# Optimization experiments

Measured on AMD Instinct MI355X. Metric: run time of the kernel, lower is better.

## Reference

```python
import jax, jax.numpy as jnp
import numpy as np

NUM_HEADS = 8
CHUNK = 64


def setup_inputs() -> dict:
    key = jax.random.key(0)
    k1, k2, k3, k4 = jax.random.split(key, 4)
    B, C, H, W = 16, 384, 64, 64
    x = jax.random.normal(k1, (B, C, H, W), dtype=jnp.float32)
    # torch nn.Linear weights are [out, in]; qkv has no bias (qkv_bias=False)
    qkv_w = jax.random.normal(k2, (3 * C, C), dtype=jnp.float32) * (C ** -0.5)
    proj_w = jax.random.normal(k3, (C, C), dtype=jnp.float32) * (C ** -0.5)
    proj_b = jax.random.normal(k4, (C,), dtype=jnp.float32) * 0.02
    return {"x": x, "qkv_w": qkv_w, "proj_w": proj_w, "proj_b": proj_b}


def reference(x, qkv_w, proj_w, proj_b):
    B, C, H, W = x.shape
    N = H * W
    nh = NUM_HEADS
    hd = C // nh
    scale = hd ** -0.5
    nc = N // CHUNK  # number of non-overlapping local blocks

    t = x.reshape(B, C, N).transpose(0, 2, 1)  # [B, N, C]
    qkv = t @ qkv_w.T  # [B, N, 3C]
    qkv = qkv.reshape(B, N, 3, nh, hd).transpose(2, 0, 3, 1, 4)  # [3, B, nh, N, hd]
    q, k, v = qkv[0], qkv[1], qkv[2]

    # block-local attention: reshape N -> (nc, CHUNK) and batch over blocks
    q = q.reshape(B, nh, nc, CHUNK, hd)
    k = k.reshape(B, nh, nc, CHUNK, hd)
    v = v.reshape(B, nh, nc, CHUNK, hd)

    scores = jnp.einsum('bhnqd,bhnkd->bhnqk', q, k) * scale  # [B,nh,nc,CHUNK,CHUNK]
    attn = jax.nn.softmax(scores, axis=-1)
    out = jnp.einsum('bhnqk,bhnkd->bhnqd', attn, v)  # [B,nh,nc,CHUNK,hd]

    out = out.reshape(B, nh, N, hd).transpose(0, 2, 1, 3).reshape(B, N, C)
    out = out @ proj_w.T + proj_b
    return out.transpose(0, 2, 1).reshape(B, C, H, W)
```

## Files before the change

kernel.cpp:

```cpp
#include <hip/hip_runtime.h>
#include <stdint.h>

#define NH 8
#define HD 48
#define CC 384
#define NN 4096
#define CK 384

typedef short short8 __attribute__((ext_vector_type(8)));
typedef float floatx4 __attribute__((ext_vector_type(4)));

__device__ inline unsigned short f32_to_bf16_bits(float f) {
    uint32_t u = __builtin_bit_cast(uint32_t, f);
    u = (u + 0x7FFFu + ((u >> 16) & 1u)) >> 16;
    return (unsigned short)u;
}
__device__ inline short8 load8(const unsigned short* p) {
    return *reinterpret_cast<const short8*>(p);
}
typedef __attribute__((address_space(1))) const void gvoid_t;
typedef __attribute__((address_space(3))) void lvoid_t;
__device__ inline void async16(const unsigned short* g, unsigned short* l) {
    __builtin_amdgcn_global_load_lds((gvoid_t*)g, (lvoid_t*)l, 16, 0, 0);
}

__global__ __launch_bounds__(256) void k_cvt(
    const float* __restrict__ src, unsigned short* __restrict__ dst, int n8)
{
    int i = blockIdx.x * 256 + threadIdx.x;
    if (i >= n8) return;
    const float* s = src + (size_t)i * 8;
    unsigned short t[8];
    #pragma unroll
    for (int j = 0; j < 8; ++j) t[j] = f32_to_bf16_bits(s[j]);
    *reinterpret_cast<short8*>(dst + (size_t)i * 8) = *reinterpret_cast<short8*>(t);
}

__global__ __launch_bounds__(256) void k_tr(
    const float* __restrict__ x, unsigned short* __restrict__ xT)
{
    __shared__ unsigned short tile[64][72];
    int bx = blockIdx.x;
    int nt = bx & 63; int rest = bx >> 6; int ct = rest % 6; int b = rest / 6;
    int c0 = ct * 64, n0 = nt * 64;
    int t = threadIdx.x;
    int nl = t & 63, w = t >> 6;
    const float* xb = x + (size_t)b * CC * NN;
    #pragma unroll
    for (int i = 0; i < 4; ++i) {
        int cl = w * 16 + i * 4;
        unsigned short u[4];
        #pragma unroll
        for (int j = 0; j < 4; ++j)
            u[j] = f32_to_bf16_bits(xb[(size_t)(c0 + cl + j) * NN + n0 + nl]);
        *reinterpret_cast<uint2*>(&tile[nl][cl]) = *reinterpret_cast<uint2*>(u);
    }
    __syncthreads();
    #pragma unroll
    for (int it = 0; it < 2; ++it) {
        int v = it * 256 + t;
        int row = v >> 3, seg = v & 7;
        *reinterpret_cast<short8*>(xT + ((size_t)b * NN + n0 + row) * CK + c0 + seg * 8) =
            load8(&tile[row][seg * 8]);
    }
}

__global__ __launch_bounds__(256) void k_qkv(
    const unsigned short* __restrict__ A,
    const unsigned short* __restrict__ W,
    unsigned short* __restrict__ QK,
    unsigned short* __restrict__ Vt)
{
    __shared__ unsigned short smem[17408];
    int bx = blockIdx.x;
    int l  = (bx & 7) * 576 + (bx >> 3);
    int tf = l % 9, tm = l / 9;
    int m0 = tm * 128, f0 = tf * 128;
    int tid = threadIdx.x, wid = tid >> 6, lane = tid & 63;
    int l15 = lane & 15, quad = lane >> 4;
    int wm = wid & 1, wn = wid >> 1;

    const unsigned short* Ab = A + (size_t)m0 * CK;
    const unsigned short* Wb = W + (size_t)f0 * CK;

    floatx4 acc[4][4] = {};

    auto stage = [&](int kt, int buf) {
        int k0 = kt * 32;
        unsigned short* Asd = smem + buf * 8192;
        unsigned short* Wsd = Asd + 4096;
        #pragma unroll
        for (int i = 0; i < 2; ++i) {
            int c = i * 256 + tid;
            int row = c >> 2;
            int sg  = (c & 3) ^ (row & 3);
            async16(Ab + (size_t)row * CK + k0 + sg * 8, Asd + (i * 256 + wid * 64) * 8);
            async16(Wb + (size_t)row * CK + k0 + sg * 8, Wsd + (i * 256 + wid * 64) * 8);
        }
    };

    stage(0, 0);
    __syncthreads();

    int sx = (quad ^ (l15 & 3)) * 8;
    int cur = 0;
    #pragma unroll
    for (int kk = 0; kk < 12; ++kk) {
        if (kk < 11) stage(kk + 1, cur ^ 1);
        unsigned short* As = smem + cur * 8192;
        unsigned short* Ws = As + 4096;
        short8 a[4], bf[4];
        #pragma unroll
        for (int i = 0; i < 4; ++i)
            a[i] = load8(As + (wm * 64 + i * 16 + l15) * 32 + sx);
        #pragma unroll
        for (int j = 0; j < 4; ++j)
            bf[j] = load8(Ws + (wn * 64 + j * 16 + l15) * 32 + sx);
        #pragma unroll
        for (int i = 0; i < 4; ++i)
            #pragma unroll
            for (int j = 0; j < 4; ++j)
                acc[i][j] = __builtin_amdgcn_mfma_f32_16x16x32_bf16(a[i], bf[j], acc[i][j], 0, 0, 0);
        __syncthreads();
        cur ^= 1;
    }

    int b = m0 >> 12, nb = m0 & 4095;
    if (tf < 6) {
        #pragma unroll
        for (int i = 0; i < 4; ++i)
            #pragma unroll
            for (int j = 0; j < 4; ++j)
                #pragma unroll
                for (int r = 0; r < 4; ++r)
                    smem[(wm * 64 + i * 16 + quad * 4 + r) * 128 + wn * 64 + j * 16 + l15] =
                        f32_to_bf16_bits(acc[i][j][r]);
        __syncthreads();
        #pragma unroll
        for (int it = 0; it < 8; ++it) {
            int c = it * 256 + tid;
            int row = c >> 4, seg = c & 15;
            *reinterpret_cast<short8*>(QK + (size_t)(m0 + row) * 768 + f0 + seg * 8) =
                load8(smem + row * 128 + seg * 8);
        }
    } else {
        #pragma unroll
        for (int i = 0; i < 4; ++i)
            #pragma unroll
            for (int j = 0; j < 4; ++j)
                #pragma unroll
                for (int r = 0; r < 4; ++r)
                    smem[(wn * 64 + j * 16 + l15) * 136 + wm * 64 + i * 16 + quad * 4 + r] =
                        f32_to_bf16_bits(acc[i][j][r]);
        __syncthreads();
        int fvb = (tf - 6) * 128;
        #pragma unroll
        for (int it = 0; it < 8; ++it) {
            int c = it * 256 + tid;
            int fl = c >> 4, seg = c & 15;
            int fv = fvb + fl;
            int h = fv / 48, d = fv - h * 48;
            *reinterpret_cast<short8*>(Vt + (((size_t)(b * 8 + h) * 48 + d) << 12) + nb + seg * 8) =
                load8(smem + fl * 136 + seg * 8);
        }
    }
}

__global__ __launch_bounds__(256) void k_attn(
    const unsigned short* __restrict__ QK,
    const unsigned short* __restrict__ Vt,
    unsigned short* __restrict__ AO)
{
    __shared__ unsigned short ql[64][72];
    __shared__ unsigned short kl[64][72];
    __shared__ unsigned short vt[48][72];
    __shared__ float          sc[64][66];
    __shared__ unsigned short pl[64][72];

    int bx = blockIdx.x;
    int cn = bx & 63, h = (bx >> 6) & 7, b = bx >> 9;
    int n0 = cn * 64;
    int tid = threadIdx.x, wid = tid >> 6, lane = tid & 63;
    int l15 = lane & 15, quad = lane >> 4;
    int m0w = wid * 16;
    int h48 = h * 48;
    size_t b4 = (size_t)b * NN + n0;

    for (int v = tid; v < 768; v += 256) {
        int mat = v / 384;
        int idx = v - mat * 384;
        int rr = idx / 6, seg = idx - rr * 6;
        uint4 val = *reinterpret_cast<const uint4*>(QK + (b4 + rr) * 768 + mat * 384 + h48 + seg * 8);
        unsigned short* dst = mat ? &kl[rr][seg * 8] : &ql[rr][seg * 8];
        *reinterpret_cast<uint4*>(dst) = val;
    }
    {
        short8 z = {};
        int v = tid;
        if (v < 256) {
            int mat = v >> 7, rr = (v >> 1) & 63, half = v & 1;
            unsigned short* dst = mat ? &kl[rr][48 + half * 8] : &ql[rr][48 + half * 8];
            *reinterpret_cast<short8*>(dst) = z;
        }
    }
    for (int v = tid; v < 384; v += 256) {
        int d = v >> 3, seg = v & 7;
        *reinterpret_cast<uint4*>(&vt[d][seg * 8]) =
            *reinterpret_cast<const uint4*>(Vt + (((size_t)(b * 8 + h) * 48 + d) << 12) + n0 + seg * 8);
    }
    __syncthreads();

    const float scale = 0.14433756729740643f;
    #pragma unroll
    for (int t = 0; t < 4; ++t) {
        floatx4 sacc = {};
        #pragma unroll
        for (int ks = 0; ks < 2; ++ks) {
            short8 a  = load8(&ql[m0w + l15][ks * 32 + quad * 8]);
            short8 bb = load8(&kl[t * 16 + l15][ks * 32 + quad * 8]);
            sacc = __builtin_amdgcn_mfma_f32_16x16x32_bf16(a, bb, sacc, 0, 0, 0);
        }
        #pragma unroll
        for (int r = 0; r < 4; ++r)
            sc[m0w + quad * 4 + r][t * 16 + l15] = sacc[r] * scale;
    }
    __syncthreads();

    {
        int row = m0w + l15;
        int jb  = quad * 16;
        float ev[16];
        #pragma unroll
        for (int jj = 0; jj < 16; ++jj) ev[jj] = sc[row][jb + jj];
        float m = ev[0];
        #pragma unroll
        for (int jj = 1; jj < 16; ++jj) m = fmaxf(m, ev[jj]);
        m = fmaxf(m, __shfl_xor(m, 16));
        m = fmaxf(m, __shfl_xor(m, 32));
        float s = 0.f;
        #pragma unroll
        for (int jj = 0; jj < 16; ++jj) { ev[jj] = __expf(ev[jj] - m); s += ev[jj]; }
        s += __shfl_xor(s, 16);
        s += __shfl_xor(s, 32);
        float inv = 1.0f / s;
        #pragma unroll
        for (int jj = 0; jj < 16; ++jj) pl[row][jb + jj] = f32_to_bf16_bits(ev[jj] * inv);
    }
    __syncthreads();

    #pragma unroll
    for (int t = 0; t < 3; ++t) {
        floatx4 oacc = {};
        #pragma unroll
        for (int ks = 0; ks < 2; ++ks) {
            short8 a  = load8(&pl[m0w + l15][ks * 32 + quad * 8]);
            short8 bb = load8(&vt[t * 16 + l15][ks * 32 + quad * 8]);
            oacc = __builtin_amdgcn_mfma_f32_16x16x32_bf16(a, bb, oacc, 0, 0, 0);
        }
        #pragma unroll
        for (int r = 0; r < 4; ++r)
            kl[m0w + quad * 4 + r][t * 16 + l15] = f32_to_bf16_bits(oacc[r]);
    }
    __syncthreads();

    for (int v = tid; v < 384; v += 256) {
        int rr = v / 6, seg = v - rr * 6;
        *reinterpret_cast<short8*>(AO + (b4 + rr) * CC + h48 + seg * 8) =
            load8(&kl[rr][seg * 8]);
    }
}

__global__ __launch_bounds__(256) void k_proj(
    const unsigned short* __restrict__ A,
    const unsigned short* __restrict__ W,
    const float* __restrict__ bias,
    float* __restrict__ out)
{
    __shared__ unsigned short smem[17408];
    float* fs = (float*)smem;
    int bx = blockIdx.x;
    int l  = (bx & 7) * 192 + (bx >> 3);
    int tf = l % 3, tm = l / 3;
    int m0 = tm * 128, f0 = tf * 128;
    int tid = threadIdx.x, wid = tid >> 6, lane = tid & 63;
    int l15 = lane & 15, quad = lane >> 4;
    int wm = wid & 1, wn = wid >> 1;

    const unsigned short* Ab = A + (size_t)m0 * CK;
    const unsigned short* Wb = W + (size_t)f0 * CK;

    floatx4 acc[4][4] = {};

    auto stage = [&](int kt, int buf) {
        int k0 = kt * 32;
        unsigned short* Asd = smem + buf * 8192;
        unsigned short* Wsd = Asd + 4096;
        #pragma unroll
        for (int i = 0; i < 2; ++i) {
            int c = i * 256 + tid;
            int row = c >> 2;
            int sg  = (c & 3) ^ (row & 3);
            async16(Ab + (size_t)row * CK + k0 + sg * 8, Asd + (i * 256 + wid * 64) * 8);
            async16(Wb + (size_t)row * CK + k0 + sg * 8, Wsd + (i * 256 + wid * 64) * 8);
        }
    };

    stage(0, 0);
    __syncthreads();

    int sx = (quad ^ (l15 & 3)) * 8;
    int cur = 0;
    #pragma unroll
    for (int kk = 0; kk < 12; ++kk) {
        if (kk < 11) stage(kk + 1, cur ^ 1);
        unsigned short* As = smem + cur * 8192;
        unsigned short* Ws = As + 4096;
        short8 a[4], bf[4];
        #pragma unroll
        for (int i = 0; i < 4; ++i)
            a[i] = load8(As + (wm * 64 + i * 16 + l15) * 32 + sx);
        #pragma unroll
        for (int j = 0; j < 4; ++j)
            bf[j] = load8(Ws + (wn * 64 + j * 16 + l15) * 32 + sx);
        #pragma unroll
        for (int i = 0; i < 4; ++i)
            #pragma unroll
            for (int j = 0; j < 4; ++j)
                acc[i][j] = __builtin_amdgcn_mfma_f32_16x16x32_bf16(a[i], bf[j], acc[i][j], 0, 0, 0);
        __syncthreads();
        cur ^= 1;
    }

    int b = m0 >> 12, nb = m0 & 4095;
    #pragma unroll
    for (int hh = 0; hh < 2; ++hh) {
        if (wn == hh) {
            #pragma unroll
            for (int j = 0; j < 4; ++j) {
                float bv = bias[f0 + hh * 64 + j * 16 + l15];
                #pragma unroll
                for (int i = 0; i < 4; ++i)
                    #pragma unroll
                    for (int r = 0; r < 4; ++r)
                        fs[(j * 16 + l15) * 132 + wm * 64 + i * 16 + quad * 4 + r] =
                            acc[i][j][r] + bv;
            }
        }
        __syncthreads();
        #pragma unroll
        for (int it = 0; it < 8; ++it) {
            int c = it * 256 + tid;
            int cl = c >> 5, seg = c & 31;
            *reinterpret_cast<float4*>(
                out + (((size_t)(b * CC + f0 + hh * 64 + cl)) << 12) + nb + seg * 4) =
                *reinterpret_cast<const float4*>(fs + cl * 132 + seg * 4);
        }
        __syncthreads();
    }
}

extern "C" void kernel_launch(void* const* d_in, const int* in_sizes, int n_in,
                              void* d_out, int out_size, void* d_ws, size_t ws_size,
                              hipStream_t stream) {
    const float* x      = (const float*)d_in[0];
    const float* qkv_w  = (const float*)d_in[1];
    const float* proj_w = (const float*)d_in[2];
    const float* proj_b = (const float*)d_in[3];
    float* out = (float*)d_out;

    const size_t nX  = (size_t)16 * CC * NN;
    const size_t nW1 = (size_t)3 * CC * CC;
    const size_t nW2 = (size_t)CC * CC;

    unsigned short* xT  = (unsigned short*)d_ws;
    unsigned short* w1b = xT  + nX;
    unsigned short* w2b = w1b + nW1;
    unsigned short* QK  = w2b + nW2;
    unsigned short* Vt  = QK  + (size_t)16 * NN * 768;
    unsigned short* AO  = Vt  + (size_t)16 * 8 * 48 * NN;

    k_tr  <<<dim3(16 * 6 * 64), dim3(256), 0, stream>>>(x, xT);
    k_cvt <<<dim3((int)(nW1 / 8 + 255) / 256), dim3(256), 0, stream>>>(qkv_w, w1b, (int)(nW1 / 8));
    k_cvt <<<dim3((int)(nW2 / 8 + 255) / 256), dim3(256), 0, stream>>>(proj_w, w2b, (int)(nW2 / 8));

    k_qkv <<<dim3(512 * 9), dim3(256), 0, stream>>>(xT, w1b, QK, Vt);
    k_attn<<<dim3(16 * 8 * 64), dim3(256), 0, stream>>>(QK, Vt, AO);
    k_proj<<<dim3(512 * 3), dim3(256), 0, stream>>>(AO, w2b, proj_b, out);
}
```

Before: 381.9 us.

## Triple-buffer GEMM K-loop with partial vmcnt waits in qkv and proj kernels

Changes the LDS staging in the QKV and output-projection GEMM kernels from double buffering to a three-buffer ring, issuing loads two K-steps ahead. Each step now waits only on the older async load group (vmcnt(4)) before a raw s_barrier, instead of a full __syncthreads that drains all outstanding loads. The aim is to hide global-to-LDS latency behind MFMA work. The cost is more LDS per block (which may lower occupancy) and reliance on exact hand-placed waitcnt counts for correctness.

```diff
diff --git a/kernel.cpp b/kernel.cpp
--- a/kernel.cpp
+++ b/kernel.cpp
@@ -71,7 +71,7 @@
     unsigned short* __restrict__ QK,
     unsigned short* __restrict__ Vt)
 {
-    __shared__ unsigned short smem[17408];
+    __shared__ unsigned short smem[24576];
     int bx = blockIdx.x;
     int l  = (bx & 7) * 576 + (bx >> 3);
     int tf = l % 9, tm = l / 9;
@@ -98,16 +98,9 @@
             async16(Wb + (size_t)row * CK + k0 + sg * 8, Wsd + (i * 256 + wid * 64) * 8);
         }
     };
-
-    stage(0, 0);
-    __syncthreads();
-
     int sx = (quad ^ (l15 & 3)) * 8;
-    int cur = 0;
-    #pragma unroll
-    for (int kk = 0; kk < 12; ++kk) {
-        if (kk < 11) stage(kk + 1, cur ^ 1);
-        unsigned short* As = smem + cur * 8192;
+    auto compute = [&](int buf) {
+        unsigned short* As = smem + buf * 8192;
         unsigned short* Ws = As + 4096;
         short8 a[4], bf[4];
         #pragma unroll
@@ -116,14 +109,41 @@
         #pragma unroll
         for (int j = 0; j < 4; ++j)
             bf[j] = load8(Ws + (wn * 64 + j * 16 + l15) * 32 + sx);
+        asm volatile("s_waitcnt lgkmcnt(0)" ::: "memory");
+        __builtin_amdgcn_sched_barrier(0);
         #pragma unroll
         for (int i = 0; i < 4; ++i)
             #pragma unroll
             for (int j = 0; j < 4; ++j)
                 acc[i][j] = __builtin_amdgcn_mfma_f32_16x16x32_bf16(a[i], bf[j], acc[i][j], 0, 0, 0);
-        __syncthreads();
-        cur ^= 1;
-    }
+    };
+
+    stage(0, 0);
+    stage(1, 1);
+    asm volatile("s_waitcnt vmcnt(4)" ::: "memory");
+    __builtin_amdgcn_sched_barrier(0);
+    __builtin_amdgcn_s_barrier();
+    __builtin_amdgcn_sched_barrier(0);
+
+    int cur = 0;
+    for (int kk = 0; kk < 10; ++kk) {
+        int nb3 = cur + 2; if (nb3 >= 3) nb3 -= 3;
+        stage(kk + 2, nb3);
+        compute(cur);
+        asm volatile("s_waitcnt vmcnt(4)" ::: "memory");
+        __builtin_amdgcn_sched_barrier(0);
+        __builtin_amdgcn_s_barrier();
+        __builtin_amdgcn_sched_barrier(0);
+        cur = cur + 1 == 3 ? 0 : cur + 1;
+    }
+    compute(cur);
+    asm volatile("s_waitcnt vmcnt(0)" ::: "memory");
+    __builtin_amdgcn_sched_barrier(0);
+    __builtin_amdgcn_s_barrier();
+    __builtin_amdgcn_sched_barrier(0);
+    cur = cur + 1 == 3 ? 0 : cur + 1;
+    compute(cur);
+    __syncthreads();
 
     int b = m0 >> 12, nb = m0 & 4095;
     if (tf < 6) {
@@ -276,7 +296,7 @@
     const float* __restrict__ bias,
     float* __restrict__ out)
 {
-    __shared__ unsigned short smem[17408];
+    __shared__ unsigned short smem[24576];
     float* fs = (float*)smem;
     int bx = blockIdx.x;
     int l  = (bx & 7) * 192 + (bx >> 3);
@@ -304,16 +324,9 @@
             async16(Wb + (size_t)row * CK + k0 + sg * 8, Wsd + (i * 256 + wid * 64) * 8);
         }
     };
-
-    stage(0, 0);
-    __syncthreads();
-
     int sx = (quad ^ (l15 & 3)) * 8;
-    int cur = 0;
-    #pragma unroll
-    for (int kk = 0; kk < 12; ++kk) {
-        if (kk < 11) stage(kk + 1, cur ^ 1);
-        unsigned short* As = smem + cur * 8192;
+    auto compute = [&](int buf) {
+        unsigned short* As = smem + buf * 8192;
         unsigned short* Ws = As + 4096;
         short8 a[4], bf[4];
         #pragma unroll
@@ -322,14 +335,41 @@
         #pragma unroll
         for (int j = 0; j < 4; ++j)
             bf[j] = load8(Ws + (wn * 64 + j * 16 + l15) * 32 + sx);
+        asm volatile("s_waitcnt lgkmcnt(0)" ::: "memory");
+        __builtin_amdgcn_sched_barrier(0);
         #pragma unroll
         for (int i = 0; i < 4; ++i)
             #pragma unroll
             for (int j = 0; j < 4; ++j)
                 acc[i][j] = __builtin_amdgcn_mfma_f32_16x16x32_bf16(a[i], bf[j], acc[i][j], 0, 0, 0);
-        __syncthreads();
-        cur ^= 1;
-    }
+    };
+
+    stage(0, 0);
+    stage(1, 1);
+    asm volatile("s_waitcnt vmcnt(4)" ::: "memory");
+    __builtin_amdgcn_sched_barrier(0);
+    __builtin_amdgcn_s_barrier();
+    __builtin_amdgcn_sched_barrier(0);
+
+    int cur = 0;
+    for (int kk = 0; kk < 10; ++kk) {
+        int nb3 = cur + 2; if (nb3 >= 3) nb3 -= 3;
+        stage(kk + 2, nb3);
+        compute(cur);
+        asm volatile("s_waitcnt vmcnt(4)" ::: "memory");
+        __builtin_amdgcn_sched_barrier(0);
+        __builtin_amdgcn_s_barrier();
+        __builtin_amdgcn_sched_barrier(0);
+        cur = cur + 1 == 3 ? 0 : cur + 1;
+    }
+    compute(cur);
+    asm volatile("s_waitcnt vmcnt(0)" ::: "memory");
+    __builtin_amdgcn_sched_barrier(0);
+    __builtin_amdgcn_s_barrier();
+    __builtin_amdgcn_sched_barrier(0);
+    cur = cur + 1 == 3 ? 0 : cur + 1;
+    compute(cur);
+    __syncthreads();
 
     int b = m0 >> 12, nb = m0 & 4095;
     #pragma unroll
```

Measured after the change: 349.3 us. -8.5%, faster.
